# Performance work log

Measured on AMD Instinct MI355X. Metric: run time of the kernel, lower is better.

Reference implementation:

```python
import jax, jax.numpy as jnp
import numpy as np

TOP_K = 6
N_EXPERTS = 64
N_GROUP = 8
TOPK_GROUP = 3
HIDDEN = 4096
BATCH, SEQ = 4, 4096


def setup_inputs() -> dict:
    key = jax.random.key(0)
    k1, k2 = jax.random.split(key)
    x = jax.random.normal(k1, (BATCH, SEQ, HIDDEN), dtype=jnp.float32)
    # kaiming_uniform_(a=sqrt(5)) on (E, H) -> U(-1/sqrt(H), 1/sqrt(H))
    bound = 1.0 / np.sqrt(HIDDEN)
    weight = jax.random.uniform(k2, (N_EXPERTS, HIDDEN), minval=-bound, maxval=bound, dtype=jnp.float32)
    return {"x": x, "weight": weight}


def reference(x, weight):
    # Flatten tokens: (B, S, H) -> (T, H)
    T = x.shape[0] * x.shape[1]
    h = x.reshape(T, HIDDEN).astype(jnp.float32)
    # Router logits and probabilities, fp32 as in the original.
    logits = jnp.einsum('th,eh->te', h, weight.astype(jnp.float32))  # (T, E)
    scores = jax.nn.softmax(logits, axis=-1)
    # Group-limited greedy: pick topk_group groups by per-group max score.
    epg = N_EXPERTS // N_GROUP
    group_max = scores.reshape(T, N_GROUP, epg).max(axis=-1)          # (T, G)
    _, gidx = jax.lax.top_k(group_max, TOPK_GROUP)                    # (T, Kg)
    group_mask = jax.nn.one_hot(gidx, N_GROUP, dtype=scores.dtype).sum(axis=1)  # (T, G)
    expert_mask = jnp.repeat(group_mask, epg, axis=-1)                # (T, E)
    masked_scores = jnp.where(expert_mask > 0, scores, 0.0)
    # Final top-k over masked scores. torch used sorted=False; jax returns
    # sorted descending -- same expert set and weights, order may differ.
    topk_weight, topk_idx = jax.lax.top_k(masked_scores, TOP_K)      # (T, k)
    return topk_idx, topk_weight
```

## Files before the change

kernel.cpp:

```cpp
#include <hip/hip_runtime.h>
#include <hip/hip_bf16.h>


#define TM     64
#define HK     128
#define PITCH  132
#define NE     64
#define NH     4096
#define KSPLIT 2
#define KHALF  (NH / KSPLIT)
#define NTOPK  6

__global__ __launch_bounds__(256, 2) void moe_gemm_kernel(
    const float* __restrict__ x, const float* __restrict__ w,
    float* __restrict__ partial, int T)
{
    __shared__ float xs[TM * PITCH];
    __shared__ float ws[NE * PITCH];

    const int tid  = threadIdx.x;
    const int tx   = tid & 15;
    const int ty   = tid >> 4;
    const int blk  = blockIdx.x;
    const int t0   = (blk >> 1) * TM;
    const int kb   = (blk & 1) * KHALF;

    float acc[4][4];
    #pragma unroll
    for (int i = 0; i < 4; ++i)
        #pragma unroll
        for (int j = 0; j < 4; ++j) acc[i][j] = 0.f;

    const int c4 = (tid & 31) << 2;
    const int r0 = tid >> 5;

    const float* xrow = xs + ty * PITCH;
    const float* wrow = ws + tx * PITCH;

    for (int k0 = 0; k0 < KHALF; k0 += HK) {
        #pragma unroll
        for (int p = 0; p < 8; ++p) {
            const int r = r0 + (p << 3);
            const float4 v = *reinterpret_cast<const float4*>(
                x + (size_t)(t0 + r) * NH + kb + k0 + c4);
            *reinterpret_cast<float4*>(&xs[r * PITCH + c4]) = v;
        }
        #pragma unroll
        for (int p = 0; p < 8; ++p) {
            const int r = r0 + (p << 3);
            const float4 v = *reinterpret_cast<const float4*>(
                w + (size_t)r * NH + kb + k0 + c4);
            *reinterpret_cast<float4*>(&ws[r * PITCH + c4]) = v;
        }
        __syncthreads();

        #pragma unroll 8
        for (int kk = 0; kk < HK; kk += 4) {
            float4 xa[4], wv[4];
            xa[0] = *reinterpret_cast<const float4*>(xrow + kk);
            xa[1] = *reinterpret_cast<const float4*>(xrow + 16 * PITCH + kk);
            xa[2] = *reinterpret_cast<const float4*>(xrow + 32 * PITCH + kk);
            xa[3] = *reinterpret_cast<const float4*>(xrow + 48 * PITCH + kk);
            wv[0] = *reinterpret_cast<const float4*>(wrow + kk);
            wv[1] = *reinterpret_cast<const float4*>(wrow + 16 * PITCH + kk);
            wv[2] = *reinterpret_cast<const float4*>(wrow + 32 * PITCH + kk);
            wv[3] = *reinterpret_cast<const float4*>(wrow + 48 * PITCH + kk);
            #pragma unroll
            for (int i = 0; i < 4; ++i)
                #pragma unroll
                for (int j = 0; j < 4; ++j) {
                    acc[i][j] = fmaf(xa[i].x, wv[j].x, acc[i][j]);
                    acc[i][j] = fmaf(xa[i].y, wv[j].y, acc[i][j]);
                    acc[i][j] = fmaf(xa[i].z, wv[j].z, acc[i][j]);
                    acc[i][j] = fmaf(xa[i].w, wv[j].w, acc[i][j]);
                }
        }
        __syncthreads();
    }

    float* pbase = partial + (size_t)(blk & 1) * T * NE;
    #pragma unroll
    for (int i = 0; i < 4; ++i)
        #pragma unroll
        for (int j = 0; j < 4; ++j)
            pbase[(size_t)(t0 + ty + (i << 4)) * NE + tx + (j << 4)] = acc[i][j];
}

__global__ __launch_bounds__(256, 4) void moe_gate_kernel(
    const float* __restrict__ partial,
    float* __restrict__ out_idx, float* __restrict__ out_w, int T)
{
    const int tid  = threadIdx.x;
    const int lane = tid & 63;
    const int wid  = tid >> 6;
    const int tb   = blockIdx.x * 32 + wid * 8;

    for (int tt = 0; tt < 8; ++tt) {
        const int t = tb + tt;
        const float logit = partial[(size_t)t * NE + lane]
                          + partial[(size_t)(T + t) * NE + lane];

        float m = logit;
        #pragma unroll
        for (int s = 32; s > 0; s >>= 1) m = fmaxf(m, __shfl_xor(m, s));
        const float ex = expf(logit - m);
        float sum = ex;
        #pragma unroll
        for (int s = 32; s > 0; s >>= 1) sum += __shfl_xor(sum, s);
        const float score = ex / sum;

        float gm = score;
        #pragma unroll
        for (int s = 4; s > 0; s >>= 1) gm = fmaxf(gm, __shfl_xor(gm, s));
        const int g = lane >> 3;

        int grank = 0;
        #pragma unroll
        for (int gg = 0; gg < 8; ++gg) {
            const float o = __shfl(gm, gg << 3);
            grank += (o > gm) || (o == gm && gg < g);
        }
        const float masked = (grank < 3) ? score : 0.0f;

        int rank = 0;
        for (int ee = 0; ee < 64; ++ee) {
            const float o = __shfl(masked, ee);
            rank += (o > masked) || (o == masked && ee < lane);
        }
        if (rank < NTOPK) {
            out_idx[t * NTOPK + rank] = (float)lane;
            out_w[t * NTOPK + rank]   = masked;
        }
    }
}

extern "C" void kernel_launch(void* const* d_in, const int* in_sizes, int n_in,
                              void* d_out, int out_size, void* d_ws, size_t ws_size,
                              hipStream_t stream) {
    const float* x = (const float*)d_in[0];
    const float* w = (const float*)d_in[1];
    const int T = in_sizes[0] / NH;
    float* outf    = (float*)d_out;
    float* out_idx = outf;
    float* out_w   = outf + (size_t)T * NTOPK;
    float* partial = (float*)d_ws;

    dim3 gg((T / TM) * KSPLIT), gb(256);
    hipLaunchKernelGGL(moe_gemm_kernel, gg, gb, 0, stream, x, w, partial, T);

    dim3 hg(T / 32), hb(256);
    hipLaunchKernelGGL(moe_gate_kernel, hg, hb, 0, stream,
                       partial, out_idx, out_w, T);
}
```

Measured before the change: 447.4 us.

## Read router weights via wave-uniform scalar loads instead of staging in LDS

Restructures the router GEMM so each thread owns one token row and each wave covers 8 experts. Weight rows are read directly from global memory at wave-uniform addresses, using readfirstlane so the loads can become scalar or broadcast, and the LDS staging of weights is removed. Blocks grow to 512 threads, and partial results are written as two float4 stores per thread. This cuts LDS traffic and footprint, but each thread now does only 8 FMAs per x load. The GEMM is compute bound, so per-FMA LDS reads of x rise and latency may be exposed on scalar loads.

```diff
diff --git a/kernel.cpp b/kernel.cpp
--- a/kernel.cpp
+++ b/kernel.cpp
@@ -11,79 +11,62 @@
 #define KHALF  (NH / KSPLIT)
 #define NTOPK  6
 
-__global__ __launch_bounds__(256, 2) void moe_gemm_kernel(
+__global__ __launch_bounds__(512, 4) void moe_gemm_kernel(
     const float* __restrict__ x, const float* __restrict__ w,
     float* __restrict__ partial, int T)
 {
     __shared__ float xs[TM * PITCH];
-    __shared__ float ws[NE * PITCH];
 
     const int tid  = threadIdx.x;
-    const int tx   = tid & 15;
-    const int ty   = tid >> 4;
+    const int lane = tid & 63;
+    const int e0   = __builtin_amdgcn_readfirstlane((tid >> 6) << 3);
     const int blk  = blockIdx.x;
     const int t0   = (blk >> 1) * TM;
     const int kb   = (blk & 1) * KHALF;
 
-    float acc[4][4];
+    float acc[8];
     #pragma unroll
-    for (int i = 0; i < 4; ++i)
-        #pragma unroll
-        for (int j = 0; j < 4; ++j) acc[i][j] = 0.f;
+    for (int j = 0; j < 8; ++j) acc[j] = 0.f;
 
     const int c4 = (tid & 31) << 2;
     const int r0 = tid >> 5;
 
-    const float* xrow = xs + ty * PITCH;
-    const float* wrow = ws + tx * PITCH;
+    const float* wr[8];
+    #pragma unroll
+    for (int j = 0; j < 8; ++j)
+        wr[j] = w + (size_t)(e0 + j) * NH + kb;
+
+    const float* xrow = xs + lane * PITCH;
 
     for (int k0 = 0; k0 < KHALF; k0 += HK) {
         #pragma unroll
-        for (int p = 0; p < 8; ++p) {
-            const int r = r0 + (p << 3);
+        for (int p = 0; p < 4; ++p) {
+            const int r = r0 + (p << 4);
             const float4 v = *reinterpret_cast<const float4*>(
                 x + (size_t)(t0 + r) * NH + kb + k0 + c4);
             *reinterpret_cast<float4*>(&xs[r * PITCH + c4]) = v;
-        }
-        #pragma unroll
-        for (int p = 0; p < 8; ++p) {
-            const int r = r0 + (p << 3);
-            const float4 v = *reinterpret_cast<const float4*>(
-                w + (size_t)r * NH + kb + k0 + c4);
-            *reinterpret_cast<float4*>(&ws[r * PITCH + c4]) = v;
         }
         __syncthreads();
 
         #pragma unroll 8
         for (int kk = 0; kk < HK; kk += 4) {
-            float4 xa[4], wv[4];
-            xa[0] = *reinterpret_cast<const float4*>(xrow + kk);
-            xa[1] = *reinterpret_cast<const float4*>(xrow + 16 * PITCH + kk);
-            xa[2] = *reinterpret_cast<const float4*>(xrow + 32 * PITCH + kk);
-            xa[3] = *reinterpret_cast<const float4*>(xrow + 48 * PITCH + kk);
-            wv[0] = *reinterpret_cast<const float4*>(wrow + kk);
-            wv[1] = *reinterpret_cast<const float4*>(wrow + 16 * PITCH + kk);
-            wv[2] = *reinterpret_cast<const float4*>(wrow + 32 * PITCH + kk);
-            wv[3] = *reinterpret_cast<const float4*>(wrow + 48 * PITCH + kk);
+            const float4 xa = *reinterpret_cast<const float4*>(xrow + kk);
             #pragma unroll
-            for (int i = 0; i < 4; ++i)
-                #pragma unroll
-                for (int j = 0; j < 4; ++j) {
-                    acc[i][j] = fmaf(xa[i].x, wv[j].x, acc[i][j]);
-                    acc[i][j] = fmaf(xa[i].y, wv[j].y, acc[i][j]);
-                    acc[i][j] = fmaf(xa[i].z, wv[j].z, acc[i][j]);
-                    acc[i][j] = fmaf(xa[i].w, wv[j].w, acc[i][j]);
-                }
+            for (int j = 0; j < 8; ++j) {
+                const float4 wv = *reinterpret_cast<const float4*>(wr[j] + k0 + kk);
+                acc[j] = fmaf(xa.x, wv.x, acc[j]);
+                acc[j] = fmaf(xa.y, wv.y, acc[j]);
+                acc[j] = fmaf(xa.z, wv.z, acc[j]);
+                acc[j] = fmaf(xa.w, wv.w, acc[j]);
+            }
         }
         __syncthreads();
     }
 
-    float* pbase = partial + (size_t)(blk & 1) * T * NE;
-    #pragma unroll
-    for (int i = 0; i < 4; ++i)
-        #pragma unroll
-        for (int j = 0; j < 4; ++j)
-            pbase[(size_t)(t0 + ty + (i << 4)) * NE + tx + (j << 4)] = acc[i][j];
+    float* pbase = partial + (size_t)(blk & 1) * T * NE
+                 + (size_t)(t0 + lane) * NE + e0;
+    *reinterpret_cast<float4*>(pbase)     = make_float4(acc[0], acc[1], acc[2], acc[3]);
+    *reinterpret_cast<float4*>(pbase + 4) = make_float4(acc[4], acc[5], acc[6], acc[7]);
 }
 
 __global__ __launch_bounds__(256, 4) void moe_gate_kernel(
@@ -145,7 +128,7 @@
     float* out_w   = outf + (size_t)T * NTOPK;
     float* partial = (float*)d_ws;
 
-    dim3 gg((T / TM) * KSPLIT), gb(256);
+    dim3 gg((T / TM) * KSPLIT), gb(512);
     hipLaunchKernelGGL(moe_gemm_kernel, gg, gb, 0, stream, x, w, partial, T);
 
     dim3 hg(T / 32), hb(256);
```

Result: slower. 655.9 us (+46.6%).
